# Kernel optimization log

Hardware: AMD Instinct MI355X
Metric: run time of the kernel (lower is better)

## Reference

```python
import jax, jax.numpy as jnp
import numpy as np

B, N, D, H = 2, 2048, 1024, 16
DK = D // H


def setup_inputs() -> dict:
    key = jax.random.key(0)
    ks = jax.random.split(key, 8)
    s = 1.0 / np.sqrt(D)  # keep projection outputs O(1)
    return {
        "x": jax.random.normal(ks[0], (B, N, D), jnp.float32),
        "alpha": jax.random.uniform(ks[1], (B, N), jnp.float32, -1.0, 1.0),
        "bias": jax.random.normal(ks[2], (B, N, N), jnp.float32) * 0.1,
        "Wq": jax.random.normal(ks[3], (D, D), jnp.float32) * s,
        "bq": jnp.zeros((D,), jnp.float32),
        "Wk": jax.random.normal(ks[4], (D, D), jnp.float32) * s,
        "bk": jnp.zeros((D,), jnp.float32),
        "Wv": jax.random.normal(ks[5], (D, D), jnp.float32) * s,
        "bv": jnp.zeros((D,), jnp.float32),
        "Wo": jax.random.normal(ks[6], (D, D), jnp.float32) * s,
        "bo": jnp.zeros((D,), jnp.float32),
    }


def reference(x, alpha, bias, Wq, bq, Wk, bk, Wv, bv, Wo, bo):
    b, n, d = x.shape
    # projections -> (B, H, N, DK)
    def split_heads(t):
        return t.reshape(b, n, H, DK).transpose(0, 2, 1, 3)

    q = split_heads(x @ Wq + bq)
    k = split_heads(x @ Wk + bk)
    v = split_heads(x @ Wv + bv)

    # salience rescale of keys/values: (B,1,N,1)
    scale = 1.0 + alpha[:, None, :, None]
    k = k * scale
    v = v * scale

    logits = jnp.einsum("bhnd,bhmd->bhnm", q, k) / np.float32(np.sqrt(DK))
    logits = logits + bias[:, None, :, :]  # broadcast over heads
    attn = jax.nn.softmax(logits, axis=-1)

    y = jnp.einsum("bhnm,bhmd->bhnd", attn, v)
    y = y.transpose(0, 2, 1, 3).reshape(b, n, d)
    return y @ Wo + bo
```

## Files before the change

### kernel.cpp

```cpp
#include <hip/hip_runtime.h>

typedef __attribute__((ext_vector_type(8))) short bf16x8;
typedef __attribute__((ext_vector_type(4))) float f32x4;

static __device__ __forceinline__ unsigned short f2bf(float f) {
    unsigned int u = __builtin_bit_cast(unsigned int, f);
    u += 0x7fffu + ((u >> 16) & 1u);
    return (unsigned short)(u >> 16);
}
static __device__ __forceinline__ float bf2f(unsigned short h) {
    unsigned int u = ((unsigned int)h) << 16;
    return __builtin_bit_cast(float, u);
}
static __device__ __forceinline__ void gload_lds16(const void* g, void* l) {
    __builtin_amdgcn_global_load_lds(
        (const __attribute__((address_space(1))) void*)g,
        (__attribute__((address_space(3))) void*)l, 16, 0, 0);
}

__global__ void convert_bf16(const float* __restrict__ src,
                             unsigned short* __restrict__ dst, int n8) {
    int i = blockIdx.x * blockDim.x + threadIdx.x;
    if (i >= n8) return;
    const float4* s4 = (const float4*)src;
    float4 a = s4[2 * i], b = s4[2 * i + 1];
    uint4 u;
    u.x = (unsigned)f2bf(a.x) | ((unsigned)f2bf(a.y) << 16);
    u.y = (unsigned)f2bf(a.z) | ((unsigned)f2bf(a.w) << 16);
    u.z = (unsigned)f2bf(b.x) | ((unsigned)f2bf(b.y) << 16);
    u.w = (unsigned)f2bf(b.z) | ((unsigned)f2bf(b.w) << 16);
    *(uint4*)(dst + 8 * (size_t)i) = u;
}

__global__ void bias_permute(const float* __restrict__ src,
                             unsigned short* __restrict__ dst) {
    int mt = blockIdx.x, qt = blockIdx.y, b = blockIdx.z;
    int tid = threadIdx.x, w = tid >> 6, lane = tid & 63;
    int quad = lane >> 4, l16 = lane & 15;
    const float* s = src + (size_t)b * 2048 * 2048;
    unsigned short* d = dst + (((size_t)(b * 16 + qt) * 32 + mt) * 8192);
    for (int e = 0; e < 2; e++) {
        unsigned short vals[16];
        for (int c = 0; c < 4; c++)
            for (int r = 0; r < 4; r++) {
                int q = qt * 128 + e * 64 + w * 16 + quad * 4 + r;
                int k = mt * 64 + c * 16 + l16;
                vals[c * 4 + r] = f2bf(s[(size_t)q * 2048 + k]);
            }
        unsigned short* o = d + ((size_t)((e * 4 + w) * 64 + lane)) * 16;
        *(bf16x8*)&o[0] = *(bf16x8*)&vals[0];
        *(bf16x8*)&o[8] = *(bf16x8*)&vals[8];
    }
}

__global__ void transpose_convert4(const float* __restrict__ W0,
                                   const float* __restrict__ W1,
                                   const float* __restrict__ W2,
                                   const float* __restrict__ W3,
                                   unsigned short* __restrict__ T0,
                                   unsigned short* __restrict__ T1,
                                   unsigned short* __restrict__ T2,
                                   unsigned short* __restrict__ T3) {
    const float* W = (blockIdx.z == 0) ? W0 : (blockIdx.z == 1) ? W1
                     : (blockIdx.z == 2) ? W2 : W3;
    unsigned short* Wt = (blockIdx.z == 0) ? T0 : (blockIdx.z == 1) ? T1
                         : (blockIdx.z == 2) ? T2 : T3;
    __shared__ float t[32][33];
    int tx = threadIdx.x, ty = threadIdx.y;
    int x0 = blockIdx.x * 32, y0 = blockIdx.y * 32;
    for (int i = 0; i < 4; i++)
        t[ty + 8 * i][tx] = W[(size_t)(y0 + ty + 8 * i) * 1024 + x0 + tx];
    __syncthreads();
    for (int i = 0; i < 4; i++)
        Wt[(size_t)(x0 + ty + 8 * i) * 1024 + y0 + tx] = f2bf(t[tx][ty + 8 * i]);
}

__launch_bounds__(256)
__global__ void gemm_qkv(const unsigned short* __restrict__ A,
                         const unsigned short* __restrict__ WqT,
                         const unsigned short* __restrict__ WkT,
                         const unsigned short* __restrict__ WvT,
                         const float* __restrict__ bq,
                         const float* __restrict__ bk,
                         const float* __restrict__ bv,
                         const float* __restrict__ alpha,
                         unsigned short* __restrict__ Qb,
                         unsigned short* __restrict__ Kb,
                         unsigned short* __restrict__ Vb) {
    int which = blockIdx.y >> 3;
    const unsigned short* Bt = (which == 0) ? WqT : (which == 1) ? WkT : WvT;
    const float* bias = (which == 0) ? bq : (which == 1) ? bk : bv;
    unsigned short* outb = (which == 0) ? Qb : (which == 1) ? Kb : Vb;

    __shared__ __align__(16) unsigned short As[128][64];
    __shared__ __align__(16) unsigned short Bs[128][64];
    int tid = threadIdx.x;
    int wave = tid >> 6, lane = tid & 63, quad = lane >> 4, l16 = lane & 15;
    int wm = wave & 1, wn = wave >> 1;
    int lrow = lane >> 3, lblk = lane & 7;
    int swz = ((lblk ^ lrow) * 8);
    int m0 = blockIdx.x * 128, n0 = (blockIdx.y & 7) * 128;
    f32x4 acc[4][4] = {};

    for (int kt = 0; kt < 16; kt++) {
        int k0 = kt * 64;
        for (int i = 0; i < 4; i++) {
            int rbase = i * 32 + wave * 8;
            gload_lds16(&A[(size_t)(m0 + rbase + lrow) * 1024 + k0 + swz],
                        &As[rbase][0]);
            gload_lds16(&Bt[(size_t)(n0 + rbase + lrow) * 1024 + k0 + swz],
                        &Bs[rbase][0]);
        }
        __syncthreads();
        for (int ks = 0; ks < 2; ks++) {
            int pblk = ((ks * 4 + quad) ^ (l16 & 7)) * 8;
            bf16x8 af[4], bf_[4];
            for (int i = 0; i < 4; i++)
                af[i] = *(const bf16x8*)&As[64 * wm + 16 * i + l16][pblk];
            for (int j = 0; j < 4; j++)
                bf_[j] = *(const bf16x8*)&Bs[64 * wn + 16 * j + l16][pblk];
            for (int i = 0; i < 4; i++)
                for (int j = 0; j < 4; j++)
                    acc[i][j] = __builtin_amdgcn_mfma_f32_16x16x32_bf16(
                        af[i], bf_[j], acc[i][j], 0, 0, 0);
        }
        __syncthreads();
    }

    for (int i = 0; i < 4; i++)
        for (int j = 0; j < 4; j++) {
            int colb = n0 + 64 * wn + 16 * j + l16;
            int h = colb >> 6, dk = colb & 63;
            for (int r = 0; r < 4; r++) {
                int row = m0 + 64 * wm + 16 * i + quad * 4 + r;
                int bb = row >> 11, nn = row & 2047;
                float v = acc[i][j][r] + bias[colb];
                float s = (which == 0) ? 0.125f : (1.0f + alpha[bb * 2048 + nn]);
                outb[((size_t)(bb * 16 + h) * 2048 + nn) * 64 + dk] = f2bf(v * s);
            }
        }
}

__launch_bounds__(256)
__global__ void gemm_out(const unsigned short* __restrict__ A,
                         const unsigned short* __restrict__ Bt,
                         const float* __restrict__ bias,
                         float* __restrict__ outf) {
    __shared__ __align__(16) unsigned short As[128][64];
    __shared__ __align__(16) unsigned short Bs[128][64];
    int tid = threadIdx.x;
    int wave = tid >> 6, lane = tid & 63, quad = lane >> 4, l16 = lane & 15;
    int wm = wave & 1, wn = wave >> 1;
    int lrow = lane >> 3, lblk = lane & 7;
    int swz = ((lblk ^ lrow) * 8);
    int m0 = blockIdx.x * 128, n0 = blockIdx.y * 128;
    f32x4 acc[4][4] = {};

    for (int kt = 0; kt < 16; kt++) {
        int k0 = kt * 64;
        for (int i = 0; i < 4; i++) {
            int rbase = i * 32 + wave * 8;
            gload_lds16(&A[(size_t)(m0 + rbase + lrow) * 1024 + k0 + swz],
                        &As[rbase][0]);
            gload_lds16(&Bt[(size_t)(n0 + rbase + lrow) * 1024 + k0 + swz],
                        &Bs[rbase][0]);
        }
        __syncthreads();
        for (int ks = 0; ks < 2; ks++) {
            int pblk = ((ks * 4 + quad) ^ (l16 & 7)) * 8;
            bf16x8 af[4], bf_[4];
            for (int i = 0; i < 4; i++)
                af[i] = *(const bf16x8*)&As[64 * wm + 16 * i + l16][pblk];
            for (int j = 0; j < 4; j++)
                bf_[j] = *(const bf16x8*)&Bs[64 * wn + 16 * j + l16][pblk];
            for (int i = 0; i < 4; i++)
                for (int j = 0; j < 4; j++)
                    acc[i][j] = __builtin_amdgcn_mfma_f32_16x16x32_bf16(
                        af[i], bf_[j], acc[i][j], 0, 0, 0);
        }
        __syncthreads();
    }

    for (int i = 0; i < 4; i++)
        for (int j = 0; j < 4; j++) {
            int colb = n0 + 64 * wn + 16 * j + l16;
            for (int r = 0; r < 4; r++) {
                int row = m0 + 64 * wm + 16 * i + quad * 4 + r;
                outf[(size_t)row * 1024 + colb] = acc[i][j][r] + bias[colb];
            }
        }
}

__global__ void transpose_v(const unsigned short* __restrict__ src,
                            unsigned short* __restrict__ dst) {
    __shared__ unsigned short t[64][72];
    int bh = blockIdx.y;
    int n0 = blockIdx.x * 64;
    src += (size_t)bh * 2048 * 64;
    dst += (size_t)bh * 64 * 2048;
    int tid = threadIdx.x;
    for (int i = 0; i < 2; i++) {
        int c = tid + i * 256;
        int row = c >> 3, k8 = (c & 7) * 8;
        bf16x8 v = *(const bf16x8*)(src + (size_t)(n0 + row) * 64 + k8);
        for (int j = 0; j < 8; j++) t[k8 + j][row] = ((unsigned short*)&v)[j];
    }
    __syncthreads();
    for (int i = 0; i < 2; i++) {
        int c = tid + i * 256;
        int dk = c >> 3, n8 = (c & 7) * 8;
        bf16x8 v;
        for (int j = 0; j < 8; j++) ((unsigned short*)&v)[j] = t[dk][n8 + j];
        *(bf16x8*)(dst + (size_t)dk * 2048 + n0 + n8) = v;
    }
}

__launch_bounds__(256)
__global__ void attn_kernel(const unsigned short* __restrict__ Q,
                            const unsigned short* __restrict__ K,
                            const unsigned short* __restrict__ Vt,
                            const unsigned short* __restrict__ biasP,
                            unsigned short* __restrict__ Y) {
    __shared__ __align__(16) unsigned short Ks[64][64];
    __shared__ __align__(16) unsigned short Vs[64][64];
    __shared__ __align__(16) unsigned short Ps[4][32][72];
    int tid = threadIdx.x;
    int wave = tid >> 6, lane = tid & 63, quad = lane >> 4, l16 = lane & 15;
    int b = blockIdx.z, h = blockIdx.y, qt = blockIdx.x, q0 = qt * 128;
    size_t headoff = (size_t)(b * 16 + h) * 2048 * 64;
    const unsigned short* Kp = K + headoff;
    const unsigned short* Vp = Vt + headoff;
    int lrow = lane >> 3, lblk = lane & 7;
    int swz = (lblk ^ lrow) * 8;

    bf16x8 aq[2][2];
    for (int e = 0; e < 2; e++) {
        const unsigned short* qp =
            Q + headoff + (size_t)(q0 + e * 64 + wave * 16 + l16) * 64;
        aq[e][0] = *(const bf16x8*)&qp[quad * 8];
        aq[e][1] = *(const bf16x8*)&qp[32 + quad * 8];
    }
    bf16x8 ones;
    for (int j = 0; j < 8; j++) ones[j] = (short)0x3F80;

    f32x4 oacc[2][4] = {};
    f32x4 lacc[2] = {};
    const unsigned short* bP = biasP + (size_t)(b * 16 + qt) * 32 * 8192;

    for (int mt = 0; mt < 32; mt++) {
        int m0 = mt * 64;
        for (int i = 0; i < 2; i++) {
            int rbase = wave * 16 + i * 8;
            gload_lds16(&Kp[(size_t)(m0 + rbase + lrow) * 64 + swz], &Ks[rbase][0]);
            gload_lds16(&Vp[(size_t)(rbase + lrow) * 2048 + m0 + swz], &Vs[rbase][0]);
        }
        const unsigned short* bt = bP + (size_t)mt * 8192;
        bf16x8 bz[2][2];
        for (int e = 0; e < 2; e++) {
            const unsigned short* p = bt + (size_t)((e * 4 + wave) * 64 + lane) * 16;
            bz[e][0] = *(const bf16x8*)&p[0];
            bz[e][1] = *(const bf16x8*)&p[8];
        }
        __syncthreads();

        f32x4 sc[2][4];
        for (int c = 0; c < 4; c++) {
            f32x4 s0 = {}, s1 = {};
            for (int ks = 0; ks < 2; ks++) {
                bf16x8 kf = *(const bf16x8*)&Ks[c * 16 + l16]
                                               [((ks * 4 + quad) ^ (l16 & 7)) * 8];
                s0 = __builtin_amdgcn_mfma_f32_16x16x32_bf16(aq[0][ks], kf, s0, 0, 0, 0);
                s1 = __builtin_amdgcn_mfma_f32_16x16x32_bf16(aq[1][ks], kf, s1, 0, 0, 0);
            }
            sc[0][c] = s0;
            sc[1][c] = s1;
        }

        for (int e = 0; e < 2; e++)
            for (int c = 0; c < 4; c++) {
                int colw = (((c * 2 + (l16 >> 3)) + quad) & 7) * 8 + (l16 & 7);
                for (int r = 0; r < 4; r++) {
                    float bb = bf2f(((unsigned short*)&bz[e][c >> 1])[(c & 1) * 4 + r]);
                    float p = __expf(fminf(sc[e][c][r] + bb, 30.f));
                    Ps[wave][e * 16 + quad * 4 + r][colw] = f2bf(p);
                }
            }

        for (int ks = 0; ks < 2; ks++) {
            int blkr = (ks * 4 + quad + (l16 >> 2)) & 7;
            bf16x8 pf0 = *(const bf16x8*)&Ps[wave][l16][blkr * 8];
            bf16x8 pf1 = *(const bf16x8*)&Ps[wave][16 + l16][blkr * 8];
            lacc[0] = __builtin_amdgcn_mfma_f32_16x16x32_bf16(pf0, ones, lacc[0], 0, 0, 0);
            lacc[1] = __builtin_amdgcn_mfma_f32_16x16x32_bf16(pf1, ones, lacc[1], 0, 0, 0);
            for (int cv = 0; cv < 4; cv++) {
                bf16x8 vf = *(const bf16x8*)&Vs[cv * 16 + l16]
                                               [((ks * 4 + quad) ^ (l16 & 7)) * 8];
                oacc[0][cv] = __builtin_amdgcn_mfma_f32_16x16x32_bf16(pf0, vf, oacc[0][cv], 0, 0, 0);
                oacc[1][cv] = __builtin_amdgcn_mfma_f32_16x16x32_bf16(pf1, vf, oacc[1][cv], 0, 0, 0);
            }
        }
        __syncthreads();
    }

    for (int e = 0; e < 2; e++) {
        float invl[4];
        for (int r = 0; r < 4; r++) invl[r] = 1.0f / lacc[e][r];
        for (int cv = 0; cv < 4; cv++)
            for (int r = 0; r < 4; r++) {
                int qrow = q0 + e * 64 + 16 * wave + quad * 4 + r;
                int d = h * 64 + cv * 16 + l16;
                Y[((size_t)b * 2048 + qrow) * 1024 + d] =
                    f2bf(oacc[e][cv][r] * invl[r]);
            }
    }
}

extern "C" void kernel_launch(void* const* d_in, const int* in_sizes, int n_in,
                              void* d_out, int out_size, void* d_ws, size_t ws_size,
                              hipStream_t stream) {
    const float* x     = (const float*)d_in[0];
    const float* alpha = (const float*)d_in[1];
    const float* bias  = (const float*)d_in[2];
    const float* Wq    = (const float*)d_in[3];
    const float* bq    = (const float*)d_in[4];
    const float* Wk    = (const float*)d_in[5];
    const float* bk    = (const float*)d_in[6];
    const float* Wv    = (const float*)d_in[7];
    const float* bv    = (const float*)d_in[8];
    const float* Wo    = (const float*)d_in[9];
    const float* bo    = (const float*)d_in[10];
    float* out = (float*)d_out;

    char* ws = (char*)d_ws;
    const size_t MB = 1048576;
    unsigned short* xb    = (unsigned short*)(ws);
    unsigned short* wqt   = (unsigned short*)(ws + 8 * MB);
    unsigned short* wkt   = (unsigned short*)(ws + 10 * MB);
    unsigned short* wvt   = (unsigned short*)(ws + 12 * MB);
    unsigned short* wot   = (unsigned short*)(ws + 14 * MB);
    unsigned short* Qb    = (unsigned short*)(ws + 16 * MB);
    unsigned short* Kb    = (unsigned short*)(ws + 24 * MB);
    unsigned short* Vb    = (unsigned short*)(ws + 32 * MB);
    unsigned short* Vtb   = (unsigned short*)(ws + 40 * MB);
    unsigned short* biasP = (unsigned short*)(ws + 48 * MB);
    unsigned short* Yb    = xb;

    convert_bf16<<<2048, 256, 0, stream>>>(x, xb, 524288);
    bias_permute<<<dim3(32, 16, 2), 256, 0, stream>>>(bias, biasP);
    transpose_convert4<<<dim3(32, 32, 4), dim3(32, 8), 0, stream>>>(
        Wq, Wk, Wv, Wo, wqt, wkt, wvt, wot);

    gemm_qkv<<<dim3(32, 24), 256, 0, stream>>>(
        xb, wqt, wkt, wvt, bq, bk, bv, alpha, Qb, Kb, Vb);

    transpose_v<<<dim3(32, 32), 256, 0, stream>>>(Vb, Vtb);

    attn_kernel<<<dim3(16, 16, 2), 256, 0, stream>>>(Qb, Kb, Vtb, biasP, Yb);

    gemm_out<<<dim3(32, 8), 256, 0, stream>>>(Yb, wot, bo, out);
}
```

Measured before the change: 272.5 us.

## Split attention over key halves, fuse V transpose into QKV GEMM, use exp2

Splits the attention key loop into two halves, doubling the block count, and adds a combine kernel that sums the fp32 partial outputs and row sums before normalising. The QKV GEMM now writes V already transposed, so the separate transpose_v kernel is removed. Bias and Q are pre-scaled by log2(e) so exp2f replaces __expf, the bias is loaded straight into the MFMA accumulator init, and the bf16 rounding of P becomes a plain truncation. The cost is extra fp32 partial traffic, one more launch, and a path that depends on workspace size.

```diff
diff --git a/kernel.cpp b/kernel.cpp
--- a/kernel.cpp
+++ b/kernel.cpp
@@ -2,6 +2,8 @@
 
 typedef __attribute__((ext_vector_type(8))) short bf16x8;
 typedef __attribute__((ext_vector_type(4))) float f32x4;
+
+#define LOG2E 1.4426950408889634f
 
 static __device__ __forceinline__ unsigned short f2bf(float f) {
     unsigned int u = __builtin_bit_cast(unsigned int, f);
@@ -45,7 +47,7 @@
             for (int r = 0; r < 4; r++) {
                 int q = qt * 128 + e * 64 + w * 16 + quad * 4 + r;
                 int k = mt * 64 + c * 16 + l16;
-                vals[c * 4 + r] = f2bf(s[(size_t)q * 2048 + k]);
+                vals[c * 4 + r] = f2bf(s[(size_t)q * 2048 + k] * LOG2E);
             }
         unsigned short* o = d + ((size_t)((e * 4 + w) * 64 + lane)) * 16;
         *(bf16x8*)&o[0] = *(bf16x8*)&vals[0];
@@ -86,11 +88,10 @@
                          const float* __restrict__ alpha,
                          unsigned short* __restrict__ Qb,
                          unsigned short* __restrict__ Kb,
-                         unsigned short* __restrict__ Vb) {
+                         unsigned short* __restrict__ Vtb) {
     int which = blockIdx.y >> 3;
     const unsigned short* Bt = (which == 0) ? WqT : (which == 1) ? WkT : WvT;
     const float* bias = (which == 0) ? bq : (which == 1) ? bk : bv;
-    unsigned short* outb = (which == 0) ? Qb : (which == 1) ? Kb : Vb;
 
     __shared__ __align__(16) unsigned short As[128][64];
     __shared__ __align__(16) unsigned short Bs[128][64];
@@ -131,12 +132,27 @@
         for (int j = 0; j < 4; j++) {
             int colb = n0 + 64 * wn + 16 * j + l16;
             int h = colb >> 6, dk = colb & 63;
-            for (int r = 0; r < 4; r++) {
-                int row = m0 + 64 * wm + 16 * i + quad * 4 + r;
-                int bb = row >> 11, nn = row & 2047;
-                float v = acc[i][j][r] + bias[colb];
-                float s = (which == 0) ? 0.125f : (1.0f + alpha[bb * 2048 + nn]);
-                outb[((size_t)(bb * 16 + h) * 2048 + nn) * 64 + dk] = f2bf(v * s);
+            int row0 = m0 + 64 * wm + 16 * i + quad * 4;
+            int bb = row0 >> 11, nn0 = row0 & 2047;
+            if (which == 2) {
+                unsigned short v4[4];
+                for (int r = 0; r < 4; r++) {
+                    float v = acc[i][j][r] + bias[colb];
+                    v4[r] = f2bf(v * (1.0f + alpha[bb * 2048 + nn0 + r]));
+                }
+                uint2 u;
+                u.x = (unsigned)v4[0] | ((unsigned)v4[1] << 16);
+                u.y = (unsigned)v4[2] | ((unsigned)v4[3] << 16);
+                *(uint2*)&Vtb[((size_t)(bb * 16 + h) * 64 + dk) * 2048 + nn0] = u;
+            } else {
+                unsigned short* outb = (which == 0) ? Qb : Kb;
+                for (int r = 0; r < 4; r++) {
+                    float v = acc[i][j][r] + bias[colb];
+                    float s = (which == 0) ? (0.125f * LOG2E)
+                                           : (1.0f + alpha[bb * 2048 + nn0 + r]);
+                    outb[((size_t)(bb * 16 + h) * 2048 + nn0 + r) * 64 + dk] =
+                        f2bf(v * s);
+                }
             }
         }
 }
@@ -191,42 +207,25 @@
         }
 }
 
-__global__ void transpose_v(const unsigned short* __restrict__ src,
-                            unsigned short* __restrict__ dst) {
-    __shared__ unsigned short t[64][72];
-    int bh = blockIdx.y;
-    int n0 = blockIdx.x * 64;
-    src += (size_t)bh * 2048 * 64;
-    dst += (size_t)bh * 64 * 2048;
-    int tid = threadIdx.x;
-    for (int i = 0; i < 2; i++) {
-        int c = tid + i * 256;
-        int row = c >> 3, k8 = (c & 7) * 8;
-        bf16x8 v = *(const bf16x8*)(src + (size_t)(n0 + row) * 64 + k8);
-        for (int j = 0; j < 8; j++) t[k8 + j][row] = ((unsigned short*)&v)[j];
-    }
-    __syncthreads();
-    for (int i = 0; i < 2; i++) {
-        int c = tid + i * 256;
-        int dk = c >> 3, n8 = (c & 7) * 8;
-        bf16x8 v;
-        for (int j = 0; j < 8; j++) ((unsigned short*)&v)[j] = t[dk][n8 + j];
-        *(bf16x8*)(dst + (size_t)dk * 2048 + n0 + n8) = v;
-    }
-}
-
-__launch_bounds__(256)
+__launch_bounds__(256, 4)
 __global__ void attn_kernel(const unsigned short* __restrict__ Q,
                             const unsigned short* __restrict__ K,
                             const unsigned short* __restrict__ Vt,
                             const unsigned short* __restrict__ biasP,
-                            unsigned short* __restrict__ Y) {
+                            unsigned short* __restrict__ Y,
+                            float* __restrict__ Opart,
+                            float* __restrict__ Lpart, int split) {
     __shared__ __align__(16) unsigned short Ks[64][64];
     __shared__ __align__(16) unsigned short Vs[64][64];
     __shared__ __align__(16) unsigned short Ps[4][32][72];
     int tid = threadIdx.x;
     int wave = tid >> 6, lane = tid & 63, quad = lane >> 4, l16 = lane & 15;
-    int b = blockIdx.z, h = blockIdx.y, qt = blockIdx.x, q0 = qt * 128;
+    int qt = blockIdx.x, h = blockIdx.y;
+    int b, mt0, mtN;
+    if (split) { b = blockIdx.z >> 1; int half = blockIdx.z & 1;
+                 mt0 = half * 16; mtN = mt0 + 16; }
+    else       { b = blockIdx.z; mt0 = 0; mtN = 32; }
+    int q0 = qt * 128;
     size_t headoff = (size_t)(b * 16 + h) * 2048 * 64;
     const unsigned short* Kp = K + headoff;
     const unsigned short* Vp = Vt + headoff;
@@ -247,7 +246,7 @@
     f32x4 lacc[2] = {};
     const unsigned short* bP = biasP + (size_t)(b * 16 + qt) * 32 * 8192;
 
-    for (int mt = 0; mt < 32; mt++) {
+    for (int mt = mt0; mt < mtN; mt++) {
         int m0 = mt * 64;
         for (int i = 0; i < 2; i++) {
             int rbase = wave * 16 + i * 8;
@@ -264,25 +263,29 @@
         __syncthreads();
 
         f32x4 sc[2][4];
+        for (int e = 0; e < 2; e++)
+            for (int c = 0; c < 4; c++) {
+                f32x4 s;
+                for (int r = 0; r < 4; r++)
+                    s[r] = bf2f(((unsigned short*)&bz[e][c >> 1])[(c & 1) * 4 + r]);
+                sc[e][c] = s;
+            }
         for (int c = 0; c < 4; c++) {
-            f32x4 s0 = {}, s1 = {};
             for (int ks = 0; ks < 2; ks++) {
                 bf16x8 kf = *(const bf16x8*)&Ks[c * 16 + l16]
                                                [((ks * 4 + quad) ^ (l16 & 7)) * 8];
-                s0 = __builtin_amdgcn_mfma_f32_16x16x32_bf16(aq[0][ks], kf, s0, 0, 0, 0);
-                s1 = __builtin_amdgcn_mfma_f32_16x16x32_bf16(aq[1][ks], kf, s1, 0, 0, 0);
-            }
-            sc[0][c] = s0;
-            sc[1][c] = s1;
+                sc[0][c] = __builtin_amdgcn_mfma_f32_16x16x32_bf16(aq[0][ks], kf, sc[0][c], 0, 0, 0);
+                sc[1][c] = __builtin_amdgcn_mfma_f32_16x16x32_bf16(aq[1][ks], kf, sc[1][c], 0, 0, 0);
+            }
         }
 
         for (int e = 0; e < 2; e++)
             for (int c = 0; c < 4; c++) {
                 int colw = (((c * 2 + (l16 >> 3)) + quad) & 7) * 8 + (l16 & 7);
                 for (int r = 0; r < 4; r++) {
-                    float bb = bf2f(((unsigned short*)&bz[e][c >> 1])[(c & 1) * 4 + r]);
-                    float p = __expf(fminf(sc[e][c][r] + bb, 30.f));
-                    Ps[wave][e * 16 + quad * 4 + r][colw] = f2bf(p);
+                    float p = exp2f(sc[e][c][r]);
+                    unsigned int u = __builtin_bit_cast(unsigned int, p);
+                    Ps[wave][e * 16 + quad * 4 + r][colw] = (unsigned short)(u >> 16);
                 }
             }
 
@@ -302,16 +305,57 @@
         __syncthreads();
     }
 
-    for (int e = 0; e < 2; e++) {
-        float invl[4];
-        for (int r = 0; r < 4; r++) invl[r] = 1.0f / lacc[e][r];
-        for (int cv = 0; cv < 4; cv++)
-            for (int r = 0; r < 4; r++) {
-                int qrow = q0 + e * 64 + 16 * wave + quad * 4 + r;
-                int d = h * 64 + cv * 16 + l16;
-                Y[((size_t)b * 2048 + qrow) * 1024 + d] =
-                    f2bf(oacc[e][cv][r] * invl[r]);
-            }
+    if (split) {
+        size_t p = ((size_t)((b * 16 + h) * 16 + qt)) * 2 + (blockIdx.z & 1);
+        float* Op = Opart + p * 8192;
+        for (int e = 0; e < 2; e++)
+            for (int cv = 0; cv < 4; cv++)
+                for (int r = 0; r < 4; r++)
+                    Op[(e * 64 + wave * 16 + quad * 4 + r) * 64 + cv * 16 + l16] =
+                        oacc[e][cv][r];
+        if (l16 == 0)
+            for (int e = 0; e < 2; e++)
+                for (int r = 0; r < 4; r++)
+                    Lpart[p * 128 + e * 64 + wave * 16 + quad * 4 + r] = lacc[e][r];
+    } else {
+        for (int e = 0; e < 2; e++) {
+            float invl[4];
+            for (int r = 0; r < 4; r++) invl[r] = 1.0f / lacc[e][r];
+            for (int cv = 0; cv < 4; cv++)
+                for (int r = 0; r < 4; r++) {
+                    int qrow = q0 + e * 64 + 16 * wave + quad * 4 + r;
+                    int d = h * 64 + cv * 16 + l16;
+                    Y[((size_t)b * 2048 + qrow) * 1024 + d] =
+                        f2bf(oacc[e][cv][r] * invl[r]);
+                }
+        }
+    }
+}
+
+__global__ void attn_combine(const float* __restrict__ Opart,
+                             const float* __restrict__ Lpart,
+                             unsigned short* __restrict__ Y) {
+    int blk = blockIdx.x;
+    int qt = blk & 15, h = (blk >> 4) & 15, b = blk >> 8;
+    const float* O0 = Opart + (size_t)blk * 2 * 8192;
+    const float* O1 = O0 + 8192;
+    const float* L0 = Lpart + (size_t)blk * 2 * 128;
+    const float* L1 = L0 + 128;
+    int t = threadIdx.x;
+    for (int i = 0; i < 8; i++) {
+        int idx4 = i * 256 + t;
+        int q = idx4 >> 4;
+        int dk = (idx4 & 15) * 4;
+        float4 a = *(const float4*)&O0[idx4 * 4];
+        float4 c = *(const float4*)&O1[idx4 * 4];
+        float inv = 1.0f / (L0[q] + L1[q]);
+        uint2 u;
+        u.x = (unsigned)f2bf((a.x + c.x) * inv) |
+              ((unsigned)f2bf((a.y + c.y) * inv) << 16);
+        u.y = (unsigned)f2bf((a.z + c.z) * inv) |
+              ((unsigned)f2bf((a.w + c.w) * inv) << 16);
+        int qrow = qt * 128 + q;
+        *(uint2*)&Y[((size_t)b * 2048 + qrow) * 1024 + h * 64 + dk] = u;
     }
 }
 
@@ -340,10 +384,12 @@
     unsigned short* wot   = (unsigned short*)(ws + 14 * MB);
     unsigned short* Qb    = (unsigned short*)(ws + 16 * MB);
     unsigned short* Kb    = (unsigned short*)(ws + 24 * MB);
-    unsigned short* Vb    = (unsigned short*)(ws + 32 * MB);
-    unsigned short* Vtb   = (unsigned short*)(ws + 40 * MB);
-    unsigned short* biasP = (unsigned short*)(ws + 48 * MB);
+    unsigned short* Vtb   = (unsigned short*)(ws + 32 * MB);
+    unsigned short* biasP = (unsigned short*)(ws + 40 * MB);
+    float*          Opart = (float*)(ws + 56 * MB);
+    float*          Lpart = (float*)(ws + 88 * MB);
     unsigned short* Yb    = xb;
+    int split = (ws_size >= 90 * MB) ? 1 : 0;
 
     convert_bf16<<<2048, 256, 0, stream>>>(x, xb, 524288);
     bias_permute<<<dim3(32, 16, 2), 256, 0, stream>>>(bias, biasP);
@@ -351,11 +397,16 @@
         Wq, Wk, Wv, Wo, wqt, wkt, wvt, wot);
 
     gemm_qkv<<<dim3(32, 24), 256, 0, stream>>>(
-        xb, wqt, wkt, wvt, bq, bk, bv, alpha, Qb, Kb, Vb);
-
-    transpose_v<<<dim3(32, 32), 256, 0, stream>>>(Vb, Vtb);
-
-    attn_kernel<<<dim3(16, 16, 2), 256, 0, stream>>>(Qb, Kb, Vtb, biasP, Yb);
+        xb, wqt, wkt, wvt, bq, bk, bv, alpha, Qb, Kb, Vtb);
+
+    if (split) {
+        attn_kernel<<<dim3(16, 16, 4), 256, 0, stream>>>(
+            Qb, Kb, Vtb, biasP, Yb, Opart, Lpart, 1);
+        attn_combine<<<512, 256, 0, stream>>>(Opart, Lpart, Yb);
+    } else {
+        attn_kernel<<<dim3(16, 16, 2), 256, 0, stream>>>(
+            Qb, Kb, Vtb, biasP, Yb, Opart, Lpart, 0);
+    }
 
     gemm_out<<<dim3(32, 8), 256, 0, stream>>>(Yb, wot, bo, out);
 }
```

Result: faster. 255.1 us (-6.4%).
